# Kernel optimization log

Measured on AMD Instinct MI355X. Metric: run time of the kernel, lower is better.

Reference implementation:

```python
import jax, jax.numpy as jnp
import numpy as np

D_MODEL = 1024
NUM_HEADS = 16
D_K = D_MODEL // NUM_HEADS


def setup_inputs() -> dict:
    key = jax.random.key(0)
    ks = jax.random.split(key, 5)
    scale = 1.0 / np.sqrt(D_MODEL)
    x = jax.random.normal(ks[0], (4, 2048, D_MODEL), dtype=jnp.float32)
    W_qkv = jax.random.normal(ks[1], (D_MODEL, 3 * D_MODEL), dtype=jnp.float32) * scale
    b_qkv = jax.random.normal(ks[2], (3 * D_MODEL,), dtype=jnp.float32) * 0.02
    W_o = jax.random.normal(ks[3], (D_MODEL, D_MODEL), dtype=jnp.float32) * scale
    b_o = jax.random.normal(ks[4], (D_MODEL,), dtype=jnp.float32) * 0.02
    return {"x": x, "W_qkv": W_qkv, "b_qkv": b_qkv, "W_o": W_o, "b_o": b_o}


def reference(x, W_qkv, b_qkv, W_o, b_o):
    B, S, _ = x.shape
    qkv = x @ W_qkv + b_qkv  # [B, S, 3*D]
    q, k, v = jnp.split(qkv, 3, axis=-1)
    # [B, H, S, d_k]
    q = q.reshape(B, S, NUM_HEADS, D_K).transpose(0, 2, 1, 3)
    k = k.reshape(B, S, NUM_HEADS, D_K).transpose(0, 2, 1, 3)
    v = v.reshape(B, S, NUM_HEADS, D_K).transpose(0, 2, 1, 3)
    scores = jnp.einsum("bhqd,bhkd->bhqk", q, k) / jnp.sqrt(jnp.float32(D_K))
    causal = jnp.tril(jnp.ones((S, S), dtype=bool))  # [S, S]
    scores = jnp.where(causal[None, None], scores, jnp.float32(-1e9))
    attn = jax.nn.softmax(scores, axis=-1)
    out = jnp.einsum("bhqk,bhkd->bhqd", attn, v)  # [B, H, S, d_k]
    out = out.transpose(0, 2, 1, 3).reshape(B, S, D_MODEL)
    return out @ W_o + b_o
```

## Files before the change

### kernel.cpp

```cpp
#include <hip/hip_runtime.h>
#include <cstdint>
#include <cstddef>

typedef __bf16 bf16x8 __attribute__((ext_vector_type(8)));
typedef __bf16 bf16x4 __attribute__((ext_vector_type(4)));
typedef short s16x4 __attribute__((ext_vector_type(4)));
typedef float f32x4 __attribute__((ext_vector_type(4)));

__device__ __forceinline__ ushort f2bf(float f) {
  union { float f; uint32_t u; } v; v.f = f;
  uint32_t r = (v.u + 0x7fffu + ((v.u >> 16) & 1u)) >> 16;
  return (ushort)r;
}

__device__ __forceinline__ float fast_exp2(float x) {
#if defined(__HIP_DEVICE_COMPILE__) && __has_builtin(__builtin_amdgcn_exp2f)
  return __builtin_amdgcn_exp2f(x);
#else
  return exp2f(x);
#endif
}

__device__ __forceinline__ f32x4 mfma16(bf16x4 a, bf16x4 b, f32x4 c) {
#if defined(__HIP_DEVICE_COMPILE__)
#if __has_builtin(__builtin_amdgcn_mfma_f32_16x16x16_bf16)
  return __builtin_amdgcn_mfma_f32_16x16x16_bf16(a, b, c, 0, 0, 0);
#else
  return __builtin_amdgcn_mfma_f32_16x16x16bf16_1k(
      __builtin_bit_cast(s16x4, a), __builtin_bit_cast(s16x4, b), c, 0, 0, 0);
#endif
#else
  (void)a; (void)b;
  return c;
#endif
}

__device__ __forceinline__ void glds16(const ushort* g, ushort* l) {
  __builtin_amdgcn_global_load_lds((const __attribute__((address_space(1))) void*)g,
                                   (__attribute__((address_space(3))) void*)l, 16, 0, 0);
}

__global__ void conv_bf16(const float4* __restrict__ in, ushort4* __restrict__ out, int n4) {
  int i = blockIdx.x * blockDim.x + threadIdx.x;
  if (i < n4) {
    float4 v = in[i];
    ushort4 o;
    o.x = f2bf(v.x); o.y = f2bf(v.y); o.z = f2bf(v.z); o.w = f2bf(v.w);
    out[i] = o;
  }
}

__global__ void transpose_f32_bf16(const float* __restrict__ in, ushort* __restrict__ out,
                                   int R, int C) {
  __shared__ ushort t[32][33];
  int c0 = blockIdx.x * 32, r0 = blockIdx.y * 32;
  int tx = threadIdx.x, ty = threadIdx.y;
#pragma unroll
  for (int i = 0; i < 4; ++i)
    t[ty + i * 8][tx] = f2bf(in[(size_t)(r0 + ty + i * 8) * C + c0 + tx]);
  __syncthreads();
#pragma unroll
  for (int i = 0; i < 4; ++i)
    out[(size_t)(c0 + ty + i * 8) * R + r0 + tx] = t[tx][ty + i * 8];
}

#define BAR8() do { asm volatile("" ::: "memory"); \
                    __builtin_amdgcn_s_barrier();  \
                    asm volatile("" ::: "memory"); } while (0)
#define VMC4()  asm volatile("s_waitcnt vmcnt(4)" ::: "memory")
#define VMC0()  asm volatile("s_waitcnt vmcnt(0)" ::: "memory")

template <int MODE>
__launch_bounds__(256, 3)
__global__ void gemm_tb(const ushort* __restrict__ A, const ushort* __restrict__ Bt,
                        const float* __restrict__ bias,
                        ushort* __restrict__ o0, ushort* __restrict__ o1,
                        ushort* __restrict__ o2, float* __restrict__ of,
                        int M, int N, int K) {
  __shared__ ushort smem[24576];
  const int NT = K >> 5;
  const int tid = threadIdx.x;
  const int wid = tid >> 6;
  const int lane = tid & 63;
  const int quad = lane >> 4;
  const int l16 = lane & 15;
  const int wm = (wid >> 1) * 64;
  const int wn = (wid & 1) * 64;

  int wg = blockIdx.y * gridDim.x + blockIdx.x;
  const int ntx = gridDim.x;
  const int cpx = (ntx * gridDim.y) >> 3;
  wg = (wg & 7) * cpx + (wg >> 3);
  const int m0 = (wg / ntx) * 128;
  const int n0 = (wg % ntx) * 128;

  const int r_l = lane >> 2;
  const int q_l = ((lane & 3) - (r_l >> 1)) & 3;
  const ushort* gA0 = A + (size_t)(m0 + wid * 32 + r_l) * K + q_l * 8;
  const ushort* gB0 = Bt + (size_t)(n0 + wid * 32 + r_l) * K + q_l * 8;
  ushort* dA0 = smem + wid * 1024 + lane * 8;
  ushort* dB0 = smem + 12288 + wid * 1024 + lane * 8;

  auto stage = [&](int t, int bs) {
    const ushort* sa = gA0 + t * 32;
    ushort* da = dA0 + bs * 4096;
    glds16(sa, da);
    glds16(sa + 16 * K, da + 512);
    const ushort* sb = gB0 + t * 32;
    ushort* db = dB0 + bs * 4096;
    glds16(sb, db);
    glds16(sb + 16 * K, db + 512);
  };

  const int slot8 = (l16 * 4 + ((quad + (l16 >> 1)) & 3)) * 8;
  const int abase = (wm >> 4) * 512 + slot8;
  const int bbase = 12288 + (wn >> 4) * 512 + slot8;

  f32x4 acc[4][4];
#pragma unroll
  for (int i = 0; i < 4; ++i)
#pragma unroll
    for (int j = 0; j < 4; ++j) acc[i][j] = (f32x4){0.f, 0.f, 0.f, 0.f};

  stage(0, 0);
  stage(1, 1);
  VMC4();
  BAR8();

  int b = 0;
  for (int t = 0; t < NT; ++t) {
    bf16x8 af[4], bfr[4];
    const int boff = b * 4096;
#pragma unroll
    for (int i = 0; i < 4; ++i)
      af[i] = *(const bf16x8*)(smem + boff + abase + i * 512);
#pragma unroll
    for (int j = 0; j < 4; ++j)
      bfr[j] = *(const bf16x8*)(smem + boff + bbase + j * 512);
    const int b2 = (b == 0) ? 2 : b - 1;
    if (t + 2 < NT) stage(t + 2, b2);
    __builtin_amdgcn_s_setprio(1);
#pragma unroll
    for (int i = 0; i < 4; ++i)
#pragma unroll
      for (int j = 0; j < 4; ++j)
        acc[i][j] = __builtin_amdgcn_mfma_f32_16x16x32_bf16(af[i], bfr[j], acc[i][j], 0, 0, 0);
    __builtin_amdgcn_s_setprio(0);
    if (t + 2 < NT) { VMC4(); } else if (t + 1 < NT) { VMC0(); }
    BAR8();
    b = (b == 2) ? 0 : b + 1;
  }

  if (MODE == 1) {
#pragma unroll
    for (int i = 0; i < 4; ++i)
#pragma unroll
      for (int j = 0; j < 4; ++j) {
        const int col = n0 + wn + j * 16 + l16;
        const float bv = bias[col];
#pragma unroll
        for (int r = 0; r < 4; ++r) {
          const int row = m0 + wm + i * 16 + quad * 4 + r;
          of[(size_t)row * N + col] = acc[i][j][r] + bv;
        }
      }
  } else {
    const int bb = m0 >> 11;
    const int s0 = m0 & 2047;
    const int wr = wid >> 1;
    const int wcol = wid & 1;
#pragma unroll
    for (int hc = 0; hc < 2; ++hc) {
      const int gc0 = n0 + hc * 64;
      const int sel = gc0 >> 10;
      const int head = (gc0 & 1023) >> 6;
      const size_t bh = (size_t)(bb * 16 + head);
      __syncthreads();
      if (wcol == hc) {
#pragma unroll
        for (int j = 0; j < 4; ++j) {
          const int dloc = j * 16 + l16;
          const float bv = bias[gc0 + dloc];
#pragma unroll
          for (int i = 0; i < 4; ++i) {
#pragma unroll
            for (int r = 0; r < 4; ++r) {
              const int R = wr * 64 + i * 16 + quad * 4 + r;
              float v = acc[i][j][r] + bv;
              if (sel == 0) v *= 0.18033688011112042f;
              const ushort u = f2bf(v);
              if (sel == 2) {
                const int lc = R >> 3;
                smem[dloc * 128 + ((lc ^ (dloc & 7)) << 3) + (R & 7)] = u;
              } else {
                smem[R * 64 + (((dloc >> 3) ^ (R & 7)) << 3) + (dloc & 7)] = u;
              }
            }
          }
        }
      }
      __syncthreads();
      if (sel != 2) {
        ushort* o = sel ? o1 : o0;
        const int R = tid >> 1;
        const int gh = tid & 1;
        ushort* dst = o + (bh * 2048 + s0 + R) * 64 + gh * 32;
        const int key = R & 7;
        const uint4* srow = (const uint4*)(smem + R * 64);
#pragma unroll
        for (int g = 0; g < 4; ++g)
          ((uint4*)dst)[g] = srow[(gh * 4 + g) ^ key];
      } else {
        const int d = tid >> 2;
        const int sq = tid & 3;
        ushort* dst = o2 + (((size_t)(bh * 32 + (s0 >> 6) + (sq >> 1))) << 12) +
                      d * 64 + (sq & 1) * 32;
        const uint4* srow = (const uint4*)(smem + d * 128);
#pragma unroll
        for (int g = 0; g < 4; ++g)
          ((uint4*)dst)[g] = srow[(sq * 4 + g) ^ (d & 7)];
      }
    }
  }
}

__launch_bounds__(256)
__global__ void attn_fused(const ushort* __restrict__ Qb, const ushort* __restrict__ Kb,
                           const ushort* __restrict__ Vt, ushort* __restrict__ Ob) {
  int wg0 = blockIdx.y * 8 + blockIdx.x;
  const int w = (wg0 & 7) * 64 + (wg0 >> 3);
  const int bh = w >> 3;
  const int pair = w & 7;
  const int tid = threadIdx.x;
  const int wid = tid >> 6;
  const int lane = tid & 63;
  const int quad = lane >> 4;
  const int l16 = lane & 15;

  __shared__ ushort Ks[2][2][64 * 32];
  __shared__ ushort Vs[2][2][64 * 32];

  const int lr = lane >> 2;
  const int jphys = lane & 3;
  const int skey = (lr >> 1) & 3;
  const int jlog = jphys ^ skey;
  const int srow = wid * 16 + lr;
  const ushort* KgL = Kb + (size_t)bh * 2048 * 64 + (size_t)srow * 64 + jlog * 8;
  const ushort* VgL = Vt + (size_t)bh * 32 * 4096 + (size_t)srow * 64 + jlog * 8;
  ushort* ldsK0[2], *ldsK1[2], *ldsV0[2], *ldsV1[2];
#pragma unroll
  for (int buf = 0; buf < 2; ++buf) {
    ldsK0[buf] = &Ks[buf][0][wid * 16 * 32] + lane * 8;
    ldsK1[buf] = &Ks[buf][1][wid * 16 * 32] + lane * 8;
    ldsV0[buf] = &Vs[buf][0][wid * 16 * 32] + lane * 8;
    ldsV1[buf] = &Vs[buf][1][wid * 16 * 32] + lane * 8;
  }
  auto stage = [&](int jt) {
    const int buf = jt & 1;
    const ushort* ks = KgL + (size_t)jt * 4096;
    const ushort* vs = VgL + (size_t)jt * 4096;
    glds16(ks, ldsK0[buf]);
    glds16(ks + 32, ldsK1[buf]);
    glds16(vs, ldsV0[buf]);
    glds16(vs + 32, ldsV1[buf]);
  };

  const int rkey = (l16 >> 1) & 3;
  const int b = bh >> 4, h = bh & 15;

  auto process = [&](int qt) {
    const int qg0 = qt * 128 + wid * 32;

    const ushort* Qg = Qb + ((size_t)bh * 2048 + qg0) * 64;
    bf16x8 qa[2][2];
#pragma unroll
    for (int f = 0; f < 2; ++f)
#pragma unroll
      for (int hh = 0; hh < 2; ++hh)
        qa[f][hh] = *(const bf16x8*)(Qg + (f * 16 + l16) * 64 + hh * 32 + quad * 8);

    f32x4 o[2][4];
    float rs[2];
#pragma unroll
    for (int f = 0; f < 2; ++f) {
      rs[f] = 0.f;
#pragma unroll
      for (int m = 0; m < 4; ++m) o[f][m] = (f32x4){0.f, 0.f, 0.f, 0.f};
    }

    const int nIt = 2 * qt + 2;
    stage(0);

    for (int jt = 0; jt < nIt; ++jt) {
      __syncthreads();
      if (jt + 1 < nIt) stage(jt + 1);

      const int kvb = jt * 64;
      if (kvb > qg0 + 31) continue;
      const int buf = jt & 1;

      f32x4 s[2][4];
      __builtin_amdgcn_s_setprio(1);
#pragma unroll
      for (int n = 0; n < 4; ++n) {
        const int koff = (n * 16 + l16) * 32 + (quad ^ rkey) * 8;
        bf16x8 kb0 = *(const bf16x8*)&Ks[buf][0][koff];
        bf16x8 kb1 = *(const bf16x8*)&Ks[buf][1][koff];
#pragma unroll
        for (int f = 0; f < 2; ++f) {
          f32x4 z = (f32x4){0.f, 0.f, 0.f, 0.f};
          z = __builtin_amdgcn_mfma_f32_16x16x32_bf16(kb0, qa[f][0], z, 0, 0, 0);
          z = __builtin_amdgcn_mfma_f32_16x16x32_bf16(kb1, qa[f][1], z, 0, 0, 0);
          s[f][n] = z;
        }
      }
      __builtin_amdgcn_s_setprio(0);

      bf16x4 p[2][4];
      if (kvb + 63 <= qg0) {
#pragma unroll
        for (int f = 0; f < 2; ++f)
#pragma unroll
          for (int n = 0; n < 4; ++n) {
            float pe[4];
#pragma unroll
            for (int r = 0; r < 4; ++r) {
              pe[r] = fast_exp2(s[f][n][r]);
              rs[f] += pe[r];
            }
            p[f][n] = (bf16x4){(__bf16)pe[0], (__bf16)pe[1], (__bf16)pe[2], (__bf16)pe[3]};
          }
      } else {
#pragma unroll
        for (int f = 0; f < 2; ++f) {
          const int qg = qg0 + f * 16 + l16;
#pragma unroll
          for (int n = 0; n < 4; ++n) {
            const int kg0 = kvb + n * 16 + quad * 4;
            float pe[4];
#pragma unroll
            for (int r = 0; r < 4; ++r) {
              float e = fast_exp2(s[f][n][r]);
              pe[r] = (kg0 + r > qg) ? 0.f : e;
              rs[f] += pe[r];
            }
            p[f][n] = (bf16x4){(__bf16)pe[0], (__bf16)pe[1], (__bf16)pe[2], (__bf16)pe[3]};
          }
        }
      }

      __builtin_amdgcn_s_setprio(1);
#pragma unroll
      for (int m = 0; m < 4; ++m) {
        const int vrow = (m * 16 + l16) * 32;
#pragma unroll
        for (int n = 0; n < 4; ++n) {
          const int clog = (n & 1) * 2 + (quad >> 1);
          const int voff = vrow + (clog ^ rkey) * 8 + (quad & 1) * 4;
          bf16x4 va = *(const bf16x4*)&Vs[buf][n >> 1][voff];
#pragma unroll
          for (int f = 0; f < 2; ++f) o[f][m] = mfma16(va, p[f][n], o[f][m]);
        }
      }
      __builtin_amdgcn_s_setprio(0);
    }

#pragma unroll
    for (int f = 0; f < 2; ++f) {
      float t = rs[f];
      t += __shfl_xor(t, 16, 64);
      t += __shfl_xor(t, 32, 64);
      const float il = 1.f / t;
      const int q = qg0 + f * 16 + l16;
      ushort* dst = Ob + ((size_t)b * 2048 + q) * 1024 + h * 64;
#pragma unroll
      for (int m = 0; m < 4; ++m) {
        ushort4 w2;
        w2.x = f2bf(o[f][m][0] * il);
        w2.y = f2bf(o[f][m][1] * il);
        w2.z = f2bf(o[f][m][2] * il);
        w2.w = f2bf(o[f][m][3] * il);
        *(ushort4*)(dst + m * 16 + quad * 4) = w2;
      }
    }
  };

  process(15 - pair);
  __syncthreads();
  process(pair);
}

extern "C" void kernel_launch(void* const* d_in, const int* in_sizes, int n_in,
                              void* d_out, int out_size, void* d_ws, size_t ws_size,
                              hipStream_t stream) {
  const float* x    = (const float*)d_in[0];
  const float* Wqkv = (const float*)d_in[1];
  const float* bqkv = (const float*)d_in[2];
  const float* Wo   = (const float*)d_in[3];
  const float* bo   = (const float*)d_in[4];
  float* out = (float*)d_out;

  char* ws = (char*)d_ws;
  size_t off = 0;
  auto alloc = [&](size_t bytes) {
    void* p = ws + off;
    off += (bytes + 255) & ~(size_t)255;
    return p;
  };
  ushort* xbf    = (ushort*)alloc((size_t)8192 * 1024 * 2);
  ushort* Wqkv_t = (ushort*)alloc((size_t)3072 * 1024 * 2);
  ushort* Wo_t   = (ushort*)alloc((size_t)1024 * 1024 * 2);
  ushort* Qb     = (ushort*)alloc((size_t)64 * 2048 * 64 * 2);
  ushort* Kb     = (ushort*)alloc((size_t)64 * 2048 * 64 * 2);
  ushort* Vb     = (ushort*)alloc((size_t)64 * 2048 * 64 * 2);
  ushort* Ab     = (ushort*)alloc((size_t)8192 * 1024 * 2);

  conv_bf16<<<dim3(8192), dim3(256), 0, stream>>>((const float4*)x, (ushort4*)xbf,
                                                  8192 * 1024 / 4);
  transpose_f32_bf16<<<dim3(96, 32), dim3(32, 8), 0, stream>>>(Wqkv, Wqkv_t, 1024, 3072);
  transpose_f32_bf16<<<dim3(32, 32), dim3(32, 8), 0, stream>>>(Wo, Wo_t, 1024, 1024);
  gemm_tb<0><<<dim3(24, 64), dim3(256), 0, stream>>>(xbf, Wqkv_t, bqkv, Qb, Kb, Vb, nullptr,
                                                     8192, 3072, 1024);
  attn_fused<<<dim3(8, 64), dim3(256), 0, stream>>>(Qb, Kb, Vb, Ab);
  gemm_tb<1><<<dim3(8, 64), dim3(256), 0, stream>>>(Ab, Wo_t, bo, nullptr, nullptr, nullptr,
                                                    out, 8192, 1024, 1024);
}
```

Before: 259.7 us.

## Fuse fp32-to-bf16 conversion of x into QKV GEMM A-tile loads

Removes the standalone conversion kernel and the bf16 copy of x. The QKV GEMM now loads fp32 rows of x into registers, converts them to bf16 and writes them into swizzled shared memory, while B still uses direct global-to-LDS loads. The two weight-transpose launches are merged into one kernel. This saves a full write and reread of an 8192x1024 bf16 tensor and one launch. In exchange, the A operand now moves through registers and needs extra waits inside the GEMM pipeline, which can reduce load/compute overlap.

```diff
diff --git a/kernel.cpp b/kernel.cpp
--- a/kernel.cpp
+++ b/kernel.cpp
@@ -40,21 +40,18 @@
                                    (__attribute__((address_space(3))) void*)l, 16, 0, 0);
 }
 
-__global__ void conv_bf16(const float4* __restrict__ in, ushort4* __restrict__ out, int n4) {
-  int i = blockIdx.x * blockDim.x + threadIdx.x;
-  if (i < n4) {
-    float4 v = in[i];
-    ushort4 o;
-    o.x = f2bf(v.x); o.y = f2bf(v.y); o.z = f2bf(v.z); o.w = f2bf(v.w);
-    out[i] = o;
-  }
-}
-
-__global__ void transpose_f32_bf16(const float* __restrict__ in, ushort* __restrict__ out,
-                                   int R, int C) {
+__global__ void prep_weights(const float* __restrict__ Wqkv, const float* __restrict__ Wo,
+                             ushort* __restrict__ Wqkv_t, ushort* __restrict__ Wo_t) {
   __shared__ ushort t[32][33];
-  int c0 = blockIdx.x * 32, r0 = blockIdx.y * 32;
-  int tx = threadIdx.x, ty = threadIdx.y;
+  const int bx = blockIdx.x;
+  const float* in;
+  ushort* out;
+  int C, c0;
+  if (bx < 96) { in = Wqkv; out = Wqkv_t; C = 3072; c0 = bx * 32; }
+  else         { in = Wo;   out = Wo_t;   C = 1024; c0 = (bx - 96) * 32; }
+  const int R = 1024;
+  const int r0 = blockIdx.y * 32;
+  const int tx = threadIdx.x, ty = threadIdx.y;
 #pragma unroll
   for (int i = 0; i < 4; ++i)
     t[ty + i * 8][tx] = f2bf(in[(size_t)(r0 + ty + i * 8) * C + c0 + tx]);
@@ -68,12 +65,14 @@
                     __builtin_amdgcn_s_barrier();  \
                     asm volatile("" ::: "memory"); } while (0)
 #define VMC4()  asm volatile("s_waitcnt vmcnt(4)" ::: "memory")
+#define VMC2()  asm volatile("s_waitcnt vmcnt(2)" ::: "memory")
 #define VMC0()  asm volatile("s_waitcnt vmcnt(0)" ::: "memory")
+#define LGKM0() asm volatile("s_waitcnt lgkmcnt(0)" ::: "memory")
 
 template <int MODE>
 __launch_bounds__(256, 3)
-__global__ void gemm_tb(const ushort* __restrict__ A, const ushort* __restrict__ Bt,
-                        const float* __restrict__ bias,
+__global__ void gemm_tb(const ushort* __restrict__ A, const float* __restrict__ Af,
+                        const ushort* __restrict__ Bt, const float* __restrict__ bias,
                         ushort* __restrict__ o0, ushort* __restrict__ o1,
                         ushort* __restrict__ o2, float* __restrict__ of,
                         int M, int N, int K) {
@@ -95,21 +94,48 @@
   const int n0 = (wg % ntx) * 128;
 
   const int r_l = lane >> 2;
+  const int q_n = lane & 3;
   const int q_l = ((lane & 3) - (r_l >> 1)) & 3;
+  const float* gAf = Af + (size_t)(m0 + wid * 32 + r_l) * K + q_n * 8;
+  const int aslot = r_l * 4 + ((q_n + (r_l >> 1)) & 3);
+  ushort* dAw = smem + wid * 1024 + aslot * 8;
   const ushort* gA0 = A + (size_t)(m0 + wid * 32 + r_l) * K + q_l * 8;
+  ushort* dA0 = smem + wid * 1024 + lane * 8;
   const ushort* gB0 = Bt + (size_t)(n0 + wid * 32 + r_l) * K + q_l * 8;
-  ushort* dA0 = smem + wid * 1024 + lane * 8;
   ushort* dB0 = smem + 12288 + wid * 1024 + lane * 8;
 
-  auto stage = [&](int t, int bs) {
+  float4 af4[2][2];
+  auto issueA = [&](int t) {
+    const float* s0 = gAf + t * 32;
+#pragma unroll
+    for (int u = 0; u < 2; ++u) {
+      af4[u][0] = *(const float4*)(s0 + u * 16 * K);
+      af4[u][1] = *(const float4*)(s0 + u * 16 * K + 4);
+    }
+  };
+  auto cvtWriteA = [&](int bs) {
+#pragma unroll
+    for (int u = 0; u < 2; ++u) {
+      bf16x8 w;
+      w[0] = (__bf16)af4[u][0].x; w[1] = (__bf16)af4[u][0].y;
+      w[2] = (__bf16)af4[u][0].z; w[3] = (__bf16)af4[u][0].w;
+      w[4] = (__bf16)af4[u][1].x; w[5] = (__bf16)af4[u][1].y;
+      w[6] = (__bf16)af4[u][1].z; w[7] = (__bf16)af4[u][1].w;
+      *(bf16x8*)(dAw + bs * 4096 + u * 512) = w;
+    }
+  };
+  auto stageB = [&](int t, int bs) {
+    const ushort* sb = gB0 + t * 32;
+    ushort* db = dB0 + bs * 4096;
+    glds16(sb, db);
+    glds16(sb + 16 * K, db + 512);
+  };
+  auto stageAB = [&](int t, int bs) {
     const ushort* sa = gA0 + t * 32;
     ushort* da = dA0 + bs * 4096;
     glds16(sa, da);
     glds16(sa + 16 * K, da + 512);
-    const ushort* sb = gB0 + t * 32;
-    ushort* db = dB0 + bs * 4096;
-    glds16(sb, db);
-    glds16(sb + 16 * K, db + 512);
+    stageB(t, bs);
   };
 
   const int slot8 = (l16 * 4 + ((quad + (l16 >> 1)) & 3)) * 8;
@@ -122,9 +148,19 @@
 #pragma unroll
     for (int j = 0; j < 4; ++j) acc[i][j] = (f32x4){0.f, 0.f, 0.f, 0.f};
 
-  stage(0, 0);
-  stage(1, 1);
-  VMC4();
+  if constexpr (MODE == 0) {
+    issueA(0); stageB(0, 0);
+    VMC0();
+    cvtWriteA(0);
+    issueA(1); stageB(1, 1);
+    VMC2();
+    cvtWriteA(1);
+    LGKM0();
+  } else {
+    stageAB(0, 0);
+    stageAB(1, 1);
+    VMC4();
+  }
   BAR8();
 
   int b = 0;
@@ -138,7 +174,11 @@
     for (int j = 0; j < 4; ++j)
       bfr[j] = *(const bf16x8*)(smem + boff + bbase + j * 512);
     const int b2 = (b == 0) ? 2 : b - 1;
-    if (t + 2 < NT) stage(t + 2, b2);
+    if constexpr (MODE == 0) {
+      if (t + 2 < NT) { issueA(t + 2); stageB(t + 2, b2); }
+    } else {
+      if (t + 2 < NT) stageAB(t + 2, b2);
+    }
     __builtin_amdgcn_s_setprio(1);
 #pragma unroll
     for (int i = 0; i < 4; ++i)
@@ -146,7 +186,12 @@
       for (int j = 0; j < 4; ++j)
         acc[i][j] = __builtin_amdgcn_mfma_f32_16x16x32_bf16(af[i], bfr[j], acc[i][j], 0, 0, 0);
     __builtin_amdgcn_s_setprio(0);
-    if (t + 2 < NT) { VMC4(); } else if (t + 1 < NT) { VMC0(); }
+    if constexpr (MODE == 0) {
+      if (t + 2 < NT) { VMC2(); cvtWriteA(b2); LGKM0(); }
+      else if (t + 1 < NT) { VMC0(); }
+    } else {
+      if (t + 2 < NT) { VMC4(); } else if (t + 1 < NT) { VMC0(); }
+    }
     BAR8();
     b = (b == 2) ? 0 : b + 1;
   }
@@ -407,7 +452,6 @@
     off += (bytes + 255) & ~(size_t)255;
     return p;
   };
-  ushort* xbf    = (ushort*)alloc((size_t)8192 * 1024 * 2);
   ushort* Wqkv_t = (ushort*)alloc((size_t)3072 * 1024 * 2);
   ushort* Wo_t   = (ushort*)alloc((size_t)1024 * 1024 * 2);
   ushort* Qb     = (ushort*)alloc((size_t)64 * 2048 * 64 * 2);
@@ -415,13 +459,11 @@
   ushort* Vb     = (ushort*)alloc((size_t)64 * 2048 * 64 * 2);
   ushort* Ab     = (ushort*)alloc((size_t)8192 * 1024 * 2);
 
-  conv_bf16<<<dim3(8192), dim3(256), 0, stream>>>((const float4*)x, (ushort4*)xbf,
-                                                  8192 * 1024 / 4);
-  transpose_f32_bf16<<<dim3(96, 32), dim3(32, 8), 0, stream>>>(Wqkv, Wqkv_t, 1024, 3072);
-  transpose_f32_bf16<<<dim3(32, 32), dim3(32, 8), 0, stream>>>(Wo, Wo_t, 1024, 1024);
-  gemm_tb<0><<<dim3(24, 64), dim3(256), 0, stream>>>(xbf, Wqkv_t, bqkv, Qb, Kb, Vb, nullptr,
-                                                     8192, 3072, 1024);
+  prep_weights<<<dim3(128, 32), dim3(32, 8), 0, stream>>>(Wqkv, Wo, Wqkv_t, Wo_t);
+  gemm_tb<0><<<dim3(24, 64), dim3(256), 0, stream>>>(nullptr, x, Wqkv_t, bqkv,
+                                                     Qb, Kb, Vb, nullptr, 8192, 3072, 1024);
   attn_fused<<<dim3(8, 64), dim3(256), 0, stream>>>(Qb, Kb, Vb, Ab);
-  gemm_tb<1><<<dim3(8, 64), dim3(256), 0, stream>>>(Ab, Wo_t, bo, nullptr, nullptr, nullptr,
-                                                    out, 8192, 1024, 1024);
-}
+  gemm_tb<1><<<dim3(8, 64), dim3(256), 0, stream>>>(Ab, nullptr, Wo_t, bo,
+                                                    nullptr, nullptr, nullptr, out,
+                                                    8192, 1024, 1024);
+}
```

Result: slower. 271.1 us (+4.4%).

## Triple-buffer attention K/V staging and merge weight transpose launches

Applied to the files above, without the earlier changes.

The attention kernel moves from double to triple buffering of K/V tiles in LDS. It prefetches two tiles ahead and waits with explicit vmcnt and a raw barrier instead of __syncthreads, so global-to-LDS loads overlap more of the compute. The two weight transpose kernels are merged into one launch to cut launch overhead. The cost is 50% more LDS per block for K/V, which may lower occupancy, and hand-tuned vmcnt counts that depend on the exact number of loads issued per stage.

```diff
diff --git a/kernel.cpp b/kernel.cpp
--- a/kernel.cpp
+++ b/kernel.cpp
@@ -50,11 +50,18 @@
   }
 }
 
-__global__ void transpose_f32_bf16(const float* __restrict__ in, ushort* __restrict__ out,
-                                   int R, int C) {
+__global__ void prep_weights(const float* __restrict__ Wqkv, const float* __restrict__ Wo,
+                             ushort* __restrict__ Wqkv_t, ushort* __restrict__ Wo_t) {
   __shared__ ushort t[32][33];
-  int c0 = blockIdx.x * 32, r0 = blockIdx.y * 32;
-  int tx = threadIdx.x, ty = threadIdx.y;
+  const int bx = blockIdx.x;
+  const float* in;
+  ushort* out;
+  int C, c0;
+  if (bx < 96) { in = Wqkv; out = Wqkv_t; C = 3072; c0 = bx * 32; }
+  else         { in = Wo;   out = Wo_t;   C = 1024; c0 = (bx - 96) * 32; }
+  const int R = 1024;
+  const int r0 = blockIdx.y * 32;
+  const int tx = threadIdx.x, ty = threadIdx.y;
 #pragma unroll
   for (int i = 0; i < 4; ++i)
     t[ty + i * 8][tx] = f2bf(in[(size_t)(r0 + ty + i * 8) * C + c0 + tx]);
@@ -237,8 +244,8 @@
   const int quad = lane >> 4;
   const int l16 = lane & 15;
 
-  __shared__ ushort Ks[2][2][64 * 32];
-  __shared__ ushort Vs[2][2][64 * 32];
+  __shared__ ushort Ks[3][2][64 * 32];
+  __shared__ ushort Vs[3][2][64 * 32];
 
   const int lr = lane >> 2;
   const int jphys = lane & 3;
@@ -247,16 +254,15 @@
   const int srow = wid * 16 + lr;
   const ushort* KgL = Kb + (size_t)bh * 2048 * 64 + (size_t)srow * 64 + jlog * 8;
   const ushort* VgL = Vt + (size_t)bh * 32 * 4096 + (size_t)srow * 64 + jlog * 8;
-  ushort* ldsK0[2], *ldsK1[2], *ldsV0[2], *ldsV1[2];
-#pragma unroll
-  for (int buf = 0; buf < 2; ++buf) {
+  ushort* ldsK0[3], *ldsK1[3], *ldsV0[3], *ldsV1[3];
+#pragma unroll
+  for (int buf = 0; buf < 3; ++buf) {
     ldsK0[buf] = &Ks[buf][0][wid * 16 * 32] + lane * 8;
     ldsK1[buf] = &Ks[buf][1][wid * 16 * 32] + lane * 8;
     ldsV0[buf] = &Vs[buf][0][wid * 16 * 32] + lane * 8;
     ldsV1[buf] = &Vs[buf][1][wid * 16 * 32] + lane * 8;
   }
-  auto stage = [&](int jt) {
-    const int buf = jt & 1;
+  auto stage = [&](int jt, int buf) {
     const ushort* ks = KgL + (size_t)jt * 4096;
     const ushort* vs = VgL + (size_t)jt * 4096;
     glds16(ks, ldsK0[buf]);
@@ -289,80 +295,84 @@
     }
 
     const int nIt = 2 * qt + 2;
-    stage(0);
-
+    stage(0, 0);
+    stage(1, 1);
+
+    int buf = 0;
     for (int jt = 0; jt < nIt; ++jt) {
-      __syncthreads();
-      if (jt + 1 < nIt) stage(jt + 1);
+      if (jt + 1 < nIt) { VMC4(); } else { VMC0(); }
+      BAR8();
+      const int b2 = (buf == 0) ? 2 : buf - 1;
+      if (jt + 2 < nIt) stage(jt + 2, b2);
 
       const int kvb = jt * 64;
-      if (kvb > qg0 + 31) continue;
-      const int buf = jt & 1;
-
-      f32x4 s[2][4];
-      __builtin_amdgcn_s_setprio(1);
-#pragma unroll
-      for (int n = 0; n < 4; ++n) {
-        const int koff = (n * 16 + l16) * 32 + (quad ^ rkey) * 8;
-        bf16x8 kb0 = *(const bf16x8*)&Ks[buf][0][koff];
-        bf16x8 kb1 = *(const bf16x8*)&Ks[buf][1][koff];
-#pragma unroll
-        for (int f = 0; f < 2; ++f) {
-          f32x4 z = (f32x4){0.f, 0.f, 0.f, 0.f};
-          z = __builtin_amdgcn_mfma_f32_16x16x32_bf16(kb0, qa[f][0], z, 0, 0, 0);
-          z = __builtin_amdgcn_mfma_f32_16x16x32_bf16(kb1, qa[f][1], z, 0, 0, 0);
-          s[f][n] = z;
-        }
-      }
-      __builtin_amdgcn_s_setprio(0);
-
-      bf16x4 p[2][4];
-      if (kvb + 63 <= qg0) {
-#pragma unroll
-        for (int f = 0; f < 2; ++f)
-#pragma unroll
-          for (int n = 0; n < 4; ++n) {
-            float pe[4];
-#pragma unroll
-            for (int r = 0; r < 4; ++r) {
-              pe[r] = fast_exp2(s[f][n][r]);
-              rs[f] += pe[r];
-            }
-            p[f][n] = (bf16x4){(__bf16)pe[0], (__bf16)pe[1], (__bf16)pe[2], (__bf16)pe[3]};
-          }
-      } else {
-#pragma unroll
-        for (int f = 0; f < 2; ++f) {
-          const int qg = qg0 + f * 16 + l16;
-#pragma unroll
-          for (int n = 0; n < 4; ++n) {
-            const int kg0 = kvb + n * 16 + quad * 4;
-            float pe[4];
-#pragma unroll
-            for (int r = 0; r < 4; ++r) {
-              float e = fast_exp2(s[f][n][r]);
-              pe[r] = (kg0 + r > qg) ? 0.f : e;
-              rs[f] += pe[r];
-            }
-            p[f][n] = (bf16x4){(__bf16)pe[0], (__bf16)pe[1], (__bf16)pe[2], (__bf16)pe[3]};
+      if (kvb <= qg0 + 31) {
+        f32x4 s[2][4];
+        __builtin_amdgcn_s_setprio(1);
+#pragma unroll
+        for (int n = 0; n < 4; ++n) {
+          const int koff = (n * 16 + l16) * 32 + (quad ^ rkey) * 8;
+          bf16x8 kb0 = *(const bf16x8*)&Ks[buf][0][koff];
+          bf16x8 kb1 = *(const bf16x8*)&Ks[buf][1][koff];
+#pragma unroll
+          for (int f = 0; f < 2; ++f) {
+            f32x4 z = (f32x4){0.f, 0.f, 0.f, 0.f};
+            z = __builtin_amdgcn_mfma_f32_16x16x32_bf16(kb0, qa[f][0], z, 0, 0, 0);
+            z = __builtin_amdgcn_mfma_f32_16x16x32_bf16(kb1, qa[f][1], z, 0, 0, 0);
+            s[f][n] = z;
           }
         }
+        __builtin_amdgcn_s_setprio(0);
+
+        bf16x4 p[2][4];
+        if (kvb + 63 <= qg0) {
+#pragma unroll
+          for (int f = 0; f < 2; ++f)
+#pragma unroll
+            for (int n = 0; n < 4; ++n) {
+              float pe[4];
+#pragma unroll
+              for (int r = 0; r < 4; ++r) {
+                pe[r] = fast_exp2(s[f][n][r]);
+                rs[f] += pe[r];
+              }
+              p[f][n] = (bf16x4){(__bf16)pe[0], (__bf16)pe[1], (__bf16)pe[2], (__bf16)pe[3]};
+            }
+        } else {
+#pragma unroll
+          for (int f = 0; f < 2; ++f) {
+            const int qg = qg0 + f * 16 + l16;
+#pragma unroll
+            for (int n = 0; n < 4; ++n) {
+              const int kg0 = kvb + n * 16 + quad * 4;
+              float pe[4];
+#pragma unroll
+              for (int r = 0; r < 4; ++r) {
+                float e = fast_exp2(s[f][n][r]);
+                pe[r] = (kg0 + r > qg) ? 0.f : e;
+                rs[f] += pe[r];
+              }
+              p[f][n] = (bf16x4){(__bf16)pe[0], (__bf16)pe[1], (__bf16)pe[2], (__bf16)pe[3]};
+            }
+          }
+        }
+
+        __builtin_amdgcn_s_setprio(1);
+#pragma unroll
+        for (int m = 0; m < 4; ++m) {
+          const int vrow = (m * 16 + l16) * 32;
+#pragma unroll
+          for (int n = 0; n < 4; ++n) {
+            const int clog = (n & 1) * 2 + (quad >> 1);
+            const int voff = vrow + (clog ^ rkey) * 8 + (quad & 1) * 4;
+            bf16x4 va = *(const bf16x4*)&Vs[buf][n >> 1][voff];
+#pragma unroll
+            for (int f = 0; f < 2; ++f) o[f][m] = mfma16(va, p[f][n], o[f][m]);
+          }
+        }
+        __builtin_amdgcn_s_setprio(0);
       }
-
-      __builtin_amdgcn_s_setprio(1);
-#pragma unroll
-      for (int m = 0; m < 4; ++m) {
-        const int vrow = (m * 16 + l16) * 32;
-#pragma unroll
-        for (int n = 0; n < 4; ++n) {
-          const int clog = (n & 1) * 2 + (quad >> 1);
-          const int voff = vrow + (clog ^ rkey) * 8 + (quad & 1) * 4;
-          bf16x4 va = *(const bf16x4*)&Vs[buf][n >> 1][voff];
-#pragma unroll
-          for (int f = 0; f < 2; ++f) o[f][m] = mfma16(va, p[f][n], o[f][m]);
-        }
-      }
-      __builtin_amdgcn_s_setprio(0);
+      buf = (buf == 2) ? 0 : buf + 1;
     }
 
 #pragma unroll
@@ -417,8 +427,7 @@
 
   conv_bf16<<<dim3(8192), dim3(256), 0, stream>>>((const float4*)x, (ushort4*)xbf,
                                                   8192 * 1024 / 4);
-  transpose_f32_bf16<<<dim3(96, 32), dim3(32, 8), 0, stream>>>(Wqkv, Wqkv_t, 1024, 3072);
-  transpose_f32_bf16<<<dim3(32, 32), dim3(32, 8), 0, stream>>>(Wo, Wo_t, 1024, 1024);
+  prep_weights<<<dim3(128, 32), dim3(32, 8), 0, stream>>>(Wqkv, Wo, Wqkv_t, Wo_t);
   gemm_tb<0><<<dim3(24, 64), dim3(256), 0, stream>>>(xbf, Wqkv_t, bqkv, Qb, Kb, Vb, nullptr,
                                                      8192, 3072, 1024);
   attn_fused<<<dim3(8, 64), dim3(256), 0, stream>>>(Qb, Kb, Vb, Ab);
```

Result: faster. 253.2 us (-2.5%).
